# Performance work log

Measured on AMD Instinct MI355X. Metric: run time of the kernel, lower is better.

## Reference

```python
import jax, jax.numpy as jnp
import numpy as np

B, S, D, H = 4, 2048, 1024, 16
DH = D // H


def setup_inputs() -> dict:
    key = jax.random.key(0)
    ks = jax.random.split(key, 12)
    scale = 1.0 / np.sqrt(D)
    inp = {
        'q': jax.random.normal(ks[0], (B, S, D), jnp.float32),
        'k': jax.random.normal(ks[1], (B, S, D), jnp.float32),
        'v': jax.random.normal(ks[2], (B, S, D), jnp.float32),
        # causal mask, broadcast over batch and heads; masked where mask == 0
        'mask': jnp.tril(jnp.ones((S, S), jnp.int32))[None, None, :, :],
        'wq': jax.random.normal(ks[3], (D, D), jnp.float32) * scale,
        'bq': jnp.zeros((D,), jnp.float32),
        'wk': jax.random.normal(ks[4], (D, D), jnp.float32) * scale,
        'bk': jnp.zeros((D,), jnp.float32),
        'wv': jax.random.normal(ks[5], (D, D), jnp.float32) * scale,
        'bv': jnp.zeros((D,), jnp.float32),
        'wo': jax.random.normal(ks[6], (D, D), jnp.float32) * scale,
        'bo': jnp.zeros((D,), jnp.float32),
    }
    return inp


def _split_heads(x):
    # [B, S, D] -> [B, H, S, DH]
    b, s, _ = x.shape
    return x.reshape(b, s, H, DH).transpose(0, 2, 1, 3)


def reference(q, k, v, mask, wq, bq, wk, bk, wv, bv, wo, bo):
    # torch Linear: y = x @ W.T + b
    qh = _split_heads(q @ wq.T + bq)
    kh = _split_heads(k @ wk.T + bk)
    vh = _split_heads(v @ wv.T + bv)
    attn = jnp.einsum('bhqd,bhkd->bhqk', qh, kh) / np.sqrt(DH)
    attn = jnp.where(mask == 0, jnp.float32(-10000.0), attn)
    attn = jax.nn.softmax(attn, axis=-1)
    out = jnp.einsum('bhqk,bhkd->bhqd', attn, vh)
    out = out.transpose(0, 2, 1, 3).reshape(q.shape[0], q.shape[1], D)
    return out @ wo.T + bo
```

## Files before the change

kernel.cpp:

```cpp
#include <hip/hip_runtime.h>
#include <hip/hip_bf16.h>

typedef __attribute__((ext_vector_type(8))) short short8;
typedef __attribute__((ext_vector_type(4))) float f32x4;
typedef __attribute__((ext_vector_type(16))) float f32x16;
typedef __attribute__((ext_vector_type(4))) unsigned short ushort4v;
typedef __attribute__((ext_vector_type(8))) unsigned short ushort8v;
typedef __attribute__((ext_vector_type(4))) unsigned int uint4v;

#define S_LEN 2048
#define DMODEL 1024
#define NHEAD 16
#define DHEAD 64
#define BATCH 4
#define NEGBIG (-1.0e30f)
#define LOG2E 1.4426950408889634f

__device__ __forceinline__ unsigned short f2bf(float f) {
  unsigned int u = __builtin_bit_cast(unsigned int, f);
  u += 0x7fffu + ((u >> 16) & 1u);
  return (unsigned short)(u >> 16);
}

__device__ __forceinline__ unsigned int pk2bf(float lo, float hi) {
  __hip_bfloat162 t = __float22bfloat162_rn(make_float2(lo, hi));
  unsigned int r;
  __builtin_memcpy(&r, &t, 4);
  return r;
}

__device__ __forceinline__ void gload16(const void* src, void* lds_dst) {
  __builtin_amdgcn_global_load_lds(
      (const __attribute__((address_space(1))) unsigned int*)src,
      (__attribute__((address_space(3))) unsigned int*)lds_dst, 16, 0, 0);
}

__global__ __launch_bounds__(256) void cvt4_kernel(
    const float* __restrict__ i0, const float* __restrict__ i1,
    const float* __restrict__ i2, const float* __restrict__ i3,
    unsigned short* __restrict__ o0, unsigned short* __restrict__ o1,
    unsigned short* __restrict__ o2, unsigned short* __restrict__ o3, int n) {
  const float* in = (blockIdx.y == 0) ? i0 : (blockIdx.y == 1) ? i1 : (blockIdx.y == 2) ? i2 : i3;
  unsigned short* out = (blockIdx.y == 0) ? o0 : (blockIdx.y == 1) ? o1 : (blockIdx.y == 2) ? o2 : o3;
  int idx = blockIdx.x * blockDim.x + threadIdx.x;
  int stride = gridDim.x * blockDim.x;
  for (int j = idx * 8; j < n; j += stride * 8) {
    float4 a = *(const float4*)(in + j);
    float4 b = *(const float4*)(in + j + 4);
    ushort8v r;
    r[0] = f2bf(a.x); r[1] = f2bf(a.y); r[2] = f2bf(a.z); r[3] = f2bf(a.w);
    r[4] = f2bf(b.x); r[5] = f2bf(b.y); r[6] = f2bf(b.z); r[7] = f2bf(b.w);
    *(ushort8v*)(out + j) = r;
  }
}

__global__ __launch_bounds__(256) void qkv_gemm_kernel(
    const float* __restrict__ Aq, const float* __restrict__ Ak, const float* __restrict__ Av,
    const unsigned short* __restrict__ Wq, const unsigned short* __restrict__ Wk,
    const unsigned short* __restrict__ Wv,
    const float* __restrict__ bq, const float* __restrict__ bk, const float* __restrict__ bv,
    unsigned short* __restrict__ oq, unsigned short* __restrict__ ok,
    unsigned short* __restrict__ ov) {
  const int z = blockIdx.z;
  const float* A = (z == 0) ? Aq : (z == 1) ? Ak : Av;
  const unsigned short* W = (z == 0) ? Wq : (z == 1) ? Wk : Wv;
  const float* bias = (z == 0) ? bq : (z == 1) ? bk : bv;
  unsigned short* out = (z == 0) ? oq : (z == 1) ? ok : ov;
  const float oscale = (z == 0) ? 0.125f * LOG2E : 1.0f;
  const int N = DMODEL, K = DMODEL;

  __shared__ char lds[32768];
  const int tid = threadIdx.x;
  const int lane = tid & 63;
  const int wv = tid >> 6;
  const int wr = wv >> 1, wc = wv & 1;
  const int l16 = lane & 15, lg = lane >> 4;

  const int nbx = N >> 7;
  const int swz = (blockIdx.x & 7) * ((int)gridDim.x >> 3) + (blockIdx.x >> 3);
  const int tm = swz / nbx, tn = swz % nbx;

  const char* Wb = (const char*)W;

  const int arow[4] = {(tid >> 3), 32 + (tid >> 3), 64 + (tid >> 3), 96 + (tid >> 3)};
  const int aslot = tid & 7;

  float4 areg[4][2];
#pragma unroll
  for (int j = 0; j < 4; ++j) {
    const float* ap = A + (size_t)(tm * 128 + arow[j]) * K + aslot * 8;
    areg[j][0] = *(const float4*)ap;
    areg[j][1] = *(const float4*)(ap + 4);
  }

  f32x4 acc[4][4] = {};

  for (int k0 = 0; k0 < K; k0 += 64) {
#pragma unroll
    for (int i = 0; i < 4; ++i) {
      int ch = wv * 4 + i;
      int r = ch * 8 + (lane >> 3);
      int cb = ((lane & 7) * 16) ^ ((r & 7) << 4);
      gload16(Wb + ((size_t)(tn * 128 + r) * K + k0) * 2 + cb, lds + 16384 + ch * 1024);
    }
#pragma unroll
    for (int j = 0; j < 4; ++j) {
      uint4v w4;
      w4[0] = pk2bf(areg[j][0].x, areg[j][0].y);
      w4[1] = pk2bf(areg[j][0].z, areg[j][0].w);
      w4[2] = pk2bf(areg[j][1].x, areg[j][1].y);
      w4[3] = pk2bf(areg[j][1].z, areg[j][1].w);
      int r = arow[j];
      *(uint4v*)(lds + r * 128 + ((aslot * 16) ^ ((r & 7) << 4))) = w4;
    }
    __syncthreads();
    if (k0 + 64 < K) {
#pragma unroll
      for (int j = 0; j < 4; ++j) {
        const float* ap = A + (size_t)(tm * 128 + arow[j]) * K + (k0 + 64) + aslot * 8;
        areg[j][0] = *(const float4*)ap;
        areg[j][1] = *(const float4*)(ap + 4);
      }
    }
#pragma unroll
    for (int ks = 0; ks < 2; ++ks) {
      const int cbase = (ks * 32 + lg * 8) * 2;
      short8 af[4], bfr[4];
#pragma unroll
      for (int m = 0; m < 4; ++m) {
        int r = wr * 64 + m * 16 + l16;
        af[m] = *(const short8*)(lds + r * 128 + (cbase ^ ((r & 7) << 4)));
      }
#pragma unroll
      for (int n = 0; n < 4; ++n) {
        int r = wc * 64 + n * 16 + l16;
        bfr[n] = *(const short8*)(lds + 16384 + r * 128 + (cbase ^ ((r & 7) << 4)));
      }
#pragma unroll
      for (int m = 0; m < 4; ++m)
#pragma unroll
        for (int n = 0; n < 4; ++n)
          acc[m][n] = __builtin_amdgcn_mfma_f32_16x16x32_bf16(af[m], bfr[n], acc[m][n], 0, 0, 0);
    }
    __syncthreads();
  }

#pragma unroll
  for (int n = 0; n < 4; ++n) {
    int gn = tn * 128 + wc * 64 + n * 16 + l16;
    float bv2 = bias[gn];
    int h = gn >> 6, dh = gn & 63;
#pragma unroll
    for (int m = 0; m < 4; ++m) {
      int gm0 = tm * 128 + wr * 64 + m * 16 + lg * 4;
      f32x4 a = acc[m][n];
      if (z < 2) {
#pragma unroll
        for (int rr = 0; rr < 4; ++rr) {
          int gm = gm0 + rr;
          int b = gm >> 11, s = gm & 2047;
          out[(((size_t)b * NHEAD + h) * S_LEN + s) * DHEAD + dh] = f2bf((a[rr] + bv2) * oscale);
        }
      } else {
        int b = gm0 >> 11, s0 = gm0 & 2047;
        ushort4v pk;
        pk[0] = f2bf(a[0] + bv2); pk[1] = f2bf(a[1] + bv2);
        pk[2] = f2bf(a[2] + bv2); pk[3] = f2bf(a[3] + bv2);
        *(ushort4v*)(out + (((size_t)b * NHEAD + h) * DHEAD + dh) * S_LEN + s0) = pk;
      }
    }
  }
}

__global__ __launch_bounds__(256) void gemm_o_kernel(
    const unsigned short* __restrict__ A, const unsigned short* __restrict__ W,
    const float* __restrict__ bias, float* __restrict__ outp, int M, int N, int K) {
  __shared__ char lds[32768];
  const int tid = threadIdx.x;
  const int lane = tid & 63;
  const int wv = tid >> 6;
  const int wr = wv >> 1, wc = wv & 1;
  const int l16 = lane & 15, lg = lane >> 4;

  const int nbx = N >> 7;
  const int nwg = gridDim.x;
  const int swz = (blockIdx.x & 7) * (nwg >> 3) + (blockIdx.x >> 3);
  const int tm = swz / nbx, tn = swz % nbx;

  const char* Ab = (const char*)A;
  const char* Wb = (const char*)W;

  f32x4 acc[4][4] = {};

  for (int k0 = 0; k0 < K; k0 += 64) {
#pragma unroll
    for (int i = 0; i < 8; ++i) {
      int ch = wv * 8 + i;
      int chl = ch & 15;
      int r = chl * 8 + (lane >> 3);
      int cb = ((lane & 7) * 16) ^ ((r & 7) << 4);
      const char* src = (ch < 16)
          ? Ab + ((size_t)(tm * 128 + r) * K + k0) * 2 + cb
          : Wb + ((size_t)(tn * 128 + r) * K + k0) * 2 + cb;
      gload16(src, lds + ch * 1024);
    }
    __syncthreads();
#pragma unroll
    for (int ks = 0; ks < 2; ++ks) {
      const int cbase = (ks * 32 + lg * 8) * 2;
      short8 af[4], bfr[4];
#pragma unroll
      for (int m = 0; m < 4; ++m) {
        int r = wr * 64 + m * 16 + l16;
        af[m] = *(const short8*)(lds + r * 128 + (cbase ^ ((r & 7) << 4)));
      }
#pragma unroll
      for (int n = 0; n < 4; ++n) {
        int r = wc * 64 + n * 16 + l16;
        bfr[n] = *(const short8*)(lds + 16384 + r * 128 + (cbase ^ ((r & 7) << 4)));
      }
#pragma unroll
      for (int m = 0; m < 4; ++m)
#pragma unroll
        for (int n = 0; n < 4; ++n)
          acc[m][n] = __builtin_amdgcn_mfma_f32_16x16x32_bf16(af[m], bfr[n], acc[m][n], 0, 0, 0);
    }
    __syncthreads();
  }

#pragma unroll
  for (int n = 0; n < 4; ++n) {
    int gn = tn * 128 + wc * 64 + n * 16 + l16;
    float bv = bias[gn];
#pragma unroll
    for (int m = 0; m < 4; ++m) {
      int gm0 = tm * 128 + wr * 64 + m * 16 + lg * 4;
      f32x4 a = acc[m][n];
#pragma unroll
      for (int rr = 0; rr < 4; ++rr)
        outp[(size_t)(gm0 + rr) * N + gn] = a[rr] + bv;
    }
  }
}

__global__ __launch_bounds__(256) void attn_kernel(
    const unsigned short* __restrict__ qh, const unsigned short* __restrict__ kh,
    const unsigned short* __restrict__ vt, unsigned short* __restrict__ aout) {
  __shared__ char lds[32768];
  const int tid = threadIdx.x;
  const int lane = tid & 63;
  const int w = tid >> 6;
  const int l31 = lane & 31;
  const int l5 = lane >> 5;
  const int bh = blockIdx.x;
  const int b = bh >> 4, h = bh & 15;

  const char* kbase = (const char*)(kh + (size_t)bh * S_LEN * DHEAD);
  const char* vbase = (const char*)(vt + (size_t)bh * S_LEN * DHEAD);
  const unsigned short* qbase = qh + (size_t)bh * S_LEN * DHEAD;

  const int la = lane >> 3, lb = lane & 7;

  const int qb = 15 - (int)blockIdx.y;
  const int q0 = qb * 128;
  const int wq0 = q0 + w * 32;
  const int qg = wq0 + l31;
  const int nt = qb * 2 + 2;

  short8 qf[4];
#pragma unroll
  for (int f = 0; f < 4; ++f)
    qf[f] = *(const short8*)(qbase + (size_t)qg * DHEAD + f * 16 + l5 * 8);

  f32x16 oa[2] = {};
  float mrun = NEGBIG, lr = 0.f;

#pragma unroll
  for (int i = 0; i < 2; ++i) {
    int ch = w * 2 + i;
    int r = ch * 8 + la;
    int cb = (lb * 16) ^ ((r & 7) << 4);
    gload16(kbase + (size_t)r * 128 + cb, lds + ch * 1024 + lane * 16);
    gload16(vbase + (size_t)r * 4096 + cb, lds + 8192 + ch * 1024 + lane * 16);
  }
  __syncthreads();
  int cur = 0;

  for (int t = 0; t < nt; ++t) {
    const int kv0 = t * 64;
    if (t + 1 < nt) {
      char* nb = lds + (cur ^ 1) * 16384;
#pragma unroll
      for (int i = 0; i < 2; ++i) {
        int ch = w * 2 + i;
        int r = ch * 8 + la;
        int cb = (lb * 16) ^ ((r & 7) << 4);
        gload16(kbase + (size_t)(kv0 + 64 + r) * 128 + cb, nb + ch * 1024 + lane * 16);
        gload16(vbase + (size_t)r * 4096 + (size_t)(kv0 + 64) * 2 + cb,
                nb + 8192 + ch * 1024 + lane * 16);
      }
    }
    if (kv0 <= wq0 + 31) {
      const char* ldk = lds + cur * 16384;
      const char* ldv = ldk + 8192;

      f32x16 sa[2] = {};
      __builtin_amdgcn_s_setprio(1);
#pragma unroll
      for (int kb2 = 0; kb2 < 2; ++kb2) {
        const int kr = kb2 * 32 + l31;
        const char* rowp = ldk + kr * 128;
        const int sw = (kr & 7) << 4;
#pragma unroll
        for (int f = 0; f < 4; ++f) {
          short8 kf = *(const short8*)(rowp + ((f * 32 + l5 * 16) ^ sw));
          sa[kb2] = __builtin_amdgcn_mfma_f32_32x32x16_bf16(kf, qf[f], sa[kb2], 0, 0, 0);
        }
      }
      __builtin_amdgcn_s_setprio(0);

      if (kv0 + 63 > wq0) {
#pragma unroll
        for (int kb2 = 0; kb2 < 2; ++kb2)
#pragma unroll
          for (int r = 0; r < 16; ++r) {
            int kgl = kv0 + kb2 * 32 + (r & 3) + 8 * (r >> 2) + 4 * l5;
            if (kgl > qg) sa[kb2][r] = NEGBIG;
          }
      }

      float pm = sa[0][0];
#pragma unroll
      for (int kb2 = 0; kb2 < 2; ++kb2)
#pragma unroll
        for (int r = 0; r < 16; ++r) pm = fmaxf(pm, sa[kb2][r]);
      pm = fmaxf(pm, __shfl_xor(pm, 32));

      if (!__all(pm <= mrun + 8.f)) {
        float mN = fmaxf(mrun, pm);
        float sc = __builtin_amdgcn_exp2f(mrun - mN);
        mrun = mN;
        lr *= sc;
        oa[0] *= sc;
        oa[1] *= sc;
      }

      float rs = 0.f;
      short8 pfrag[4];
#pragma unroll
      for (int kb2 = 0; kb2 < 2; ++kb2) {
        unsigned int wpk[8];
#pragma unroll
        for (int i = 0; i < 8; ++i) {
          float p0 = __builtin_amdgcn_exp2f(sa[kb2][2 * i] - mrun);
          float p1 = __builtin_amdgcn_exp2f(sa[kb2][2 * i + 1] - mrun);
          rs += p0 + p1;
          wpk[i] = pk2bf(p0, p1);
        }
#pragma unroll
        for (int g = 0; g < 2; ++g) {
          unsigned int o0 = l5 ? wpk[4 * g + 2] : wpk[4 * g];
          unsigned int o1 = l5 ? wpk[4 * g + 3] : wpk[4 * g + 1];
          unsigned int s0 = l5 ? wpk[4 * g] : wpk[4 * g + 2];
          unsigned int s1 = l5 ? wpk[4 * g + 1] : wpk[4 * g + 3];
          unsigned int r0 = (unsigned int)__shfl_xor((int)s0, 32);
          unsigned int r1 = (unsigned int)__shfl_xor((int)s1, 32);
          uint4v fw;
          fw[0] = l5 ? r0 : o0;
          fw[1] = l5 ? r1 : o1;
          fw[2] = l5 ? o0 : r0;
          fw[3] = l5 ? o1 : r1;
          pfrag[kb2 * 2 + g] = __builtin_bit_cast(short8, fw);
        }
      }
      rs += __shfl_xor(rs, 32);
      lr += rs;

      __builtin_amdgcn_s_setprio(1);
#pragma unroll
      for (int db = 0; db < 2; ++db) {
        const int vr = db * 32 + l31;
        const char* rowp = ldv + vr * 128;
        const int sw = (vr & 7) << 4;
#pragma unroll
        for (int f = 0; f < 4; ++f) {
          short8 vf = *(const short8*)(rowp + ((f * 32 + l5 * 16) ^ sw));
          oa[db] = __builtin_amdgcn_mfma_f32_32x32x16_bf16(vf, pfrag[f], oa[db], 0, 0, 0);
        }
      }
      __builtin_amdgcn_s_setprio(0);
    }
    __syncthreads();
    cur ^= 1;
  }

  float rl = 1.0f / lr;
  unsigned short* obase = aout + ((size_t)(b * S_LEN + qg)) * DMODEL + h * DHEAD;
#pragma unroll
  for (int db = 0; db < 2; ++db)
#pragma unroll
    for (int rq = 0; rq < 4; ++rq) {
      ushort4v pk;
#pragma unroll
      for (int j = 0; j < 4; ++j)
        pk[j] = f2bf(oa[db][rq * 4 + j] * rl);
      *(ushort4v*)(obase + db * 32 + 8 * rq + 4 * l5) = pk;
    }
}

extern "C" void kernel_launch(void* const* d_in, const int* in_sizes, int n_in,
                              void* d_out, int out_size, void* d_ws, size_t ws_size,
                              hipStream_t stream) {
  (void)in_sizes; (void)n_in; (void)out_size; (void)ws_size;
  const float* q  = (const float*)d_in[0];
  const float* k  = (const float*)d_in[1];
  const float* v  = (const float*)d_in[2];
  const float* wq = (const float*)d_in[4];
  const float* bq = (const float*)d_in[5];
  const float* wk = (const float*)d_in[6];
  const float* bk = (const float*)d_in[7];
  const float* wv = (const float*)d_in[8];
  const float* bv = (const float*)d_in[9];
  const float* wo = (const float*)d_in[10];
  const float* bo = (const float*)d_in[11];

  const size_t NACT = (size_t)BATCH * S_LEN * DMODEL;
  const size_t NW = (size_t)DMODEL * DMODEL;
  unsigned short* wqb = (unsigned short*)d_ws;
  unsigned short* wkb = wqb + NW;
  unsigned short* wvb = wkb + NW;
  unsigned short* wob = wvb + NW;
  unsigned short* qhb = wob + NW;
  unsigned short* khb = qhb + NACT;
  unsigned short* vtb = khb + NACT;
  unsigned short* aout = vtb + NACT;

  dim3 blk(256);
  cvt4_kernel<<<dim3(512, 4), blk, 0, stream>>>(wq, wk, wv, wo, wqb, wkb, wvb, wob, (int)NW);

  const int M = BATCH * S_LEN, N = DMODEL, K = DMODEL;
  const int grid = (M / 128) * (N / 128);
  qkv_gemm_kernel<<<dim3(grid, 1, 3), blk, 0, stream>>>(
      q, k, v, wqb, wkb, wvb, bq, bk, bv, qhb, khb, vtb);

  attn_kernel<<<dim3(64, 16), blk, 0, stream>>>(qhb, khb, vtb, aout);

  gemm_o_kernel<<<grid, blk, 0, stream>>>(aout, wob, bo, (float*)d_out, M, N, K);
}
```

Before: 180.5 us.

## Load fp32 activations directly to LDS and convert to bf16 at fragment read

The QKV projection kernel used to load fp32 activation tiles into registers, convert them to bf16 and write them to LDS, prefetching the next tile into registers. It now issues direct global-to-LDS async copies of the raw fp32 tile, with LDS grown to 48KB, and converts to bf16 when building each MFMA fragment. This removes the register staging and the VGPR pressure of the prefetch. In exchange it doubles LDS traffic and footprint for A, repeats the conversion for every wave that reads a row, and drops the register-level overlap of the next A load with compute.

After: 191.4 us. +6.1%, slower.

```diff
diff --git a/kernel.cpp b/kernel.cpp
--- a/kernel.cpp
+++ b/kernel.cpp
@@ -69,7 +69,7 @@
   const float oscale = (z == 0) ? 0.125f * LOG2E : 1.0f;
   const int N = DMODEL, K = DMODEL;
 
-  __shared__ char lds[32768];
+  __shared__ char lds[49152];
   const int tid = threadIdx.x;
   const int lane = tid & 63;
   const int wv = tid >> 6;
@@ -80,61 +80,50 @@
   const int swz = (blockIdx.x & 7) * ((int)gridDim.x >> 3) + (blockIdx.x >> 3);
   const int tm = swz / nbx, tn = swz % nbx;
 
+  const char* Ab = (const char*)A;
   const char* Wb = (const char*)W;
 
-  const int arow[4] = {(tid >> 3), 32 + (tid >> 3), 64 + (tid >> 3), 96 + (tid >> 3)};
-  const int aslot = tid & 7;
-
-  float4 areg[4][2];
-#pragma unroll
-  for (int j = 0; j < 4; ++j) {
-    const float* ap = A + (size_t)(tm * 128 + arow[j]) * K + aslot * 8;
-    areg[j][0] = *(const float4*)ap;
-    areg[j][1] = *(const float4*)(ap + 4);
-  }
-
   f32x4 acc[4][4] = {};
 
   for (int k0 = 0; k0 < K; k0 += 64) {
+#pragma unroll
+    for (int i = 0; i < 8; ++i) {
+      int c = i * 256 + tid;
+      int r = c >> 4;
+      int cb = ((c & 15) * 16) ^ ((r & 7) << 4);
+      gload16(Ab + ((size_t)(tm * 128 + r) * K + k0) * 4 + cb, lds + c * 16);
+    }
 #pragma unroll
     for (int i = 0; i < 4; ++i) {
       int ch = wv * 4 + i;
       int r = ch * 8 + (lane >> 3);
       int cb = ((lane & 7) * 16) ^ ((r & 7) << 4);
-      gload16(Wb + ((size_t)(tn * 128 + r) * K + k0) * 2 + cb, lds + 16384 + ch * 1024);
-    }
-#pragma unroll
-    for (int j = 0; j < 4; ++j) {
-      uint4v w4;
-      w4[0] = pk2bf(areg[j][0].x, areg[j][0].y);
-      w4[1] = pk2bf(areg[j][0].z, areg[j][0].w);
-      w4[2] = pk2bf(areg[j][1].x, areg[j][1].y);
-      w4[3] = pk2bf(areg[j][1].z, areg[j][1].w);
-      int r = arow[j];
-      *(uint4v*)(lds + r * 128 + ((aslot * 16) ^ ((r & 7) << 4))) = w4;
+      gload16(Wb + ((size_t)(tn * 128 + r) * K + k0) * 2 + cb, lds + 32768 + ch * 1024);
     }
     __syncthreads();
-    if (k0 + 64 < K) {
-#pragma unroll
-      for (int j = 0; j < 4; ++j) {
-        const float* ap = A + (size_t)(tm * 128 + arow[j]) * K + (k0 + 64) + aslot * 8;
-        areg[j][0] = *(const float4*)ap;
-        areg[j][1] = *(const float4*)(ap + 4);
-      }
-    }
 #pragma unroll
     for (int ks = 0; ks < 2; ++ks) {
-      const int cbase = (ks * 32 + lg * 8) * 2;
+      const int cb32 = ks * 128 + lg * 32;
+      const int cb16 = (ks * 32 + lg * 8) * 2;
       short8 af[4], bfr[4];
 #pragma unroll
       for (int m = 0; m < 4; ++m) {
         int r = wr * 64 + m * 16 + l16;
-        af[m] = *(const short8*)(lds + r * 128 + (cbase ^ ((r & 7) << 4)));
+        const char* rp = lds + r * 256;
+        const int sw = (r & 7) << 4;
+        f32x4 a0 = *(const f32x4*)(rp + (cb32 ^ sw));
+        f32x4 a1 = *(const f32x4*)(rp + ((cb32 + 16) ^ sw));
+        uint4v w4;
+        w4[0] = pk2bf(a0[0], a0[1]);
+        w4[1] = pk2bf(a0[2], a0[3]);
+        w4[2] = pk2bf(a1[0], a1[1]);
+        w4[3] = pk2bf(a1[2], a1[3]);
+        af[m] = __builtin_bit_cast(short8, w4);
       }
 #pragma unroll
       for (int n = 0; n < 4; ++n) {
         int r = wc * 64 + n * 16 + l16;
-        bfr[n] = *(const short8*)(lds + 16384 + r * 128 + (cbase ^ ((r & 7) << 4)));
+        bfr[n] = *(const short8*)(lds + 32768 + r * 128 + (cb16 ^ ((r & 7) << 4)));
       }
 #pragma unroll
       for (int m = 0; m < 4; ++m)
```
